# Kernel tuning notes

Hardware: AMD Instinct MI355X
Metric: run time of the kernel (lower is better)

Reference implementation:

```python
import jax, jax.numpy as jnp
import numpy as np

T, D, E, K, F, SF = 4096, 1024, 8, 2, 1024, 1024  # tokens, d_model, experts, top_k, moe_ff, shared_ff


def setup_inputs() -> dict:
    key = jax.random.key(0)
    ks = jax.random.split(key, 10)
    hidden_states = jax.random.normal(ks[0], (T, D), jnp.float32)
    # balanced expert assignment: the fused kernel's get_split_sizes assumes tokens
    # split evenly across experts after permute_tokens, so exactly T*K/E per expert
    flat = jnp.arange(T * K) % E
    flat = jax.random.permutation(ks[1], flat)
    topk_indices = flat.reshape(T, K).astype(jnp.int32)
    w = jax.random.uniform(ks[2], (T, K), jnp.float32)
    topk_weights = w / w.sum(-1, keepdims=True)  # norm_topk_prob
    s = 0.02
    w_gate = jax.random.normal(ks[3], (E, D, F), jnp.float32) * s
    w_up = jax.random.normal(ks[4], (E, D, F), jnp.float32) * s
    w_down = jax.random.normal(ks[5], (E, F, D), jnp.float32) * s
    sw_gate = jax.random.normal(ks[6], (D, SF), jnp.float32) * s
    sw_up = jax.random.normal(ks[7], (D, SF), jnp.float32) * s
    sw_down = jax.random.normal(ks[8], (SF, D), jnp.float32) * s
    shared_gate_w = jax.random.normal(ks[9], (D, 1), jnp.float32) * s
    return dict(hidden_states=hidden_states, topk_weights=topk_weights,
                w_gate=w_gate, w_up=w_up, w_down=w_down,
                sw_gate=sw_gate, sw_up=sw_up, sw_down=sw_down,
                shared_gate_w=shared_gate_w, topk_indices=topk_indices)


def _silu(x):
    return x * jax.nn.sigmoid(x)


def reference(hidden_states, topk_weights, w_gate, w_up, w_down,
              sw_gate, sw_up, sw_down, shared_gate_w, topk_indices):
    t, d = hidden_states.shape
    e = w_gate.shape[0]
    k = topk_indices.shape[1]
    c = (t * k) // e  # tokens per expert (balanced split, as in get_split_sizes)

    # permute_tokens: replicate each token top_k times and sort by expert id
    flat_idx = topk_indices.reshape(-1)                    # [t*k]
    order = jnp.argsort(flat_idx)                          # dispatch permutation
    x_rep = jnp.repeat(hidden_states, k, axis=0)           # [t*k, d]
    xs = x_rep[order].reshape(e, c, d)                     # grouped per-expert

    # per-expert gated MLP (grouped GEMMs)
    h = _silu(jnp.einsum('ecd,edf->ecf', xs, w_gate)) * jnp.einsum('ecd,edf->ecf', xs, w_up)
    y = jnp.einsum('ecf,efd->ecd', h, w_down).reshape(t * k, d)

    # unpermute_tokens + weighted combine over top_k
    y = y[jnp.argsort(order)].reshape(t, k, d)
    out = (y * topk_weights[..., None]).sum(axis=1)        # [t, d]

    # shared expert with sigmoid gate
    s = jnp.einsum('tf,fd->td', _silu(hidden_states @ sw_gate) * (hidden_states @ sw_up), sw_down)
    g = jax.nn.sigmoid(hidden_states @ shared_gate_w)      # [t, 1]
    return (out + g * s).astype(hidden_states.dtype)
```

## Files before the change

kernel.cpp:

```cpp
#include <hip/hip_runtime.h>
#include <hip/hip_bf16.h>
#include <cstdint>
#include <cstddef>

#define TTOK 4096
#define DM   1024
#define NE   8
#define KTOP 2
#define FFD  1024
#define CPER 1024
#define MROWS 12288

typedef __attribute__((ext_vector_type(8))) short frag8;
typedef __attribute__((ext_vector_type(4))) float f32x4;

static __device__ __forceinline__ unsigned short f2bf(float f) {
  unsigned int u = __float_as_uint(f);
  u += 0x7fff + ((u >> 16) & 1);
  return (unsigned short)(u >> 16);
}
static __device__ __forceinline__ float bf2f(unsigned short u) {
  return __uint_as_float((unsigned int)u << 16);
}

static __device__ __forceinline__ void gld_lds16(const unsigned short* g, unsigned short* l) {
  __builtin_amdgcn_global_load_lds(
      (const __attribute__((address_space(1))) unsigned int*)g,
      (__attribute__((address_space(3))) unsigned int*)l,
      16, 0, 0);
}

static __device__ __forceinline__ int lds_slot(int r, int cs) {
  return r * 4 + (cs ^ ((r >> 1) & 3));
}

static __device__ __forceinline__ void stage_tile(const unsigned short* __restrict__ src,
                                                  int row0, int k0,
                                                  unsigned short* lds, int tid) {
#pragma unroll
  for (int it = 0; it < 2; ++it) {
    int seg = it * 256 + tid;
    int r = seg >> 2;
    int cs = (seg & 3) ^ ((r >> 1) & 3);
    gld_lds16(src + (size_t)(row0 + r) * 1024 + k0 + cs * 8, lds + seg * 8);
  }
}

__global__ void perm_kernel(const int* __restrict__ idx, int* __restrict__ cnt,
                            int* __restrict__ rowdst, int* __restrict__ inv) {
  int i = blockIdx.x * 256 + threadIdx.x;
  int e = idx[i];
  int pos = atomicAdd(&cnt[e], 1);
  int j = e * CPER + pos;
  rowdst[j] = i >> 1;
  inv[i] = j;
}

__global__ void pack_kernel(const float* __restrict__ x, const int* __restrict__ rowdst,
                            unsigned short* __restrict__ xall) {
  int j = blockIdx.x;
  int t = (j < 8192) ? rowdst[j] : (j - 8192);
  int c = threadIdx.x;
  float4 v = ((const float4*)(x + (size_t)t * 1024))[c];
  ushort4 o;
  o.x = f2bf(v.x); o.y = f2bf(v.y); o.z = f2bf(v.z); o.w = f2bf(v.w);
  ((ushort4*)(xall + (size_t)j * 1024))[c] = o;
}

__global__ void transw_kernel(const float* __restrict__ wg, const float* __restrict__ wu,
                              const float* __restrict__ wd, const float* __restrict__ sg,
                              const float* __restrict__ su, const float* __restrict__ sd,
                              unsigned short* __restrict__ owg, unsigned short* __restrict__ owu,
                              unsigned short* __restrict__ owd) {
  int z = blockIdx.z;
  const float* src; unsigned short* dst;
  if (z < 8)       { src = wg + (size_t)z * 1048576;        dst = owg + (size_t)z * 1048576; }
  else if (z < 16) { src = wu + (size_t)(z - 8) * 1048576;  dst = owu + (size_t)(z - 8) * 1048576; }
  else if (z < 24) { src = wd + (size_t)(z - 16) * 1048576; dst = owd + (size_t)(z - 16) * 1048576; }
  else if (z == 24){ src = sg; dst = owg + (size_t)8 * 1048576; }
  else if (z == 25){ src = su; dst = owu + (size_t)8 * 1048576; }
  else             { src = sd; dst = owd + (size_t)8 * 1048576; }
  __shared__ float tile[32][33];
  int bx = blockIdx.x * 32;
  int by = blockIdx.y * 32;
  int tx = threadIdx.x, ty = threadIdx.y;
#pragma unroll
  for (int i = 0; i < 4; ++i)
    tile[ty + 8 * i][tx] = src[(size_t)(by + ty + 8 * i) * 1024 + bx + tx];
  __syncthreads();
#pragma unroll
  for (int i = 0; i < 4; ++i)
    dst[(size_t)(bx + ty + 8 * i) * 1024 + by + tx] = f2bf(tile[tx][ty + 8 * i]);
}

__global__ void gate_kernel(const float* __restrict__ x, const float* __restrict__ gw,
                            float* __restrict__ g) {
  int t = blockIdx.x * 4 + (threadIdx.x >> 6);
  int lane = threadIdx.x & 63;
  const float4* xr = (const float4*)(x + (size_t)t * 1024);
  const float4* wr = (const float4*)gw;
  float s = 0.f;
#pragma unroll
  for (int c = lane; c < 256; c += 64) {
    float4 a = xr[c], b = wr[c];
    s += a.x * b.x + a.y * b.y + a.z * b.z + a.w * b.w;
  }
#pragma unroll
  for (int off = 32; off; off >>= 1) s += __shfl_down(s, off);
  if (lane == 0) g[t] = 1.f / (1.f + __expf(-s));
}

static __device__ __forceinline__ int eid_of(int y) { return (y < 64) ? (y >> 3) : 8; }

__global__ __launch_bounds__(256, 2) void gemm1_kernel(
    const unsigned short* __restrict__ A, const unsigned short* __restrict__ Bg,
    const unsigned short* __restrict__ Bu, unsigned short* __restrict__ H) {
  __shared__ __align__(16) unsigned short As[128 * 32];
  __shared__ __align__(16) unsigned short Bgs[128 * 32];
  __shared__ __align__(16) unsigned short Bus[128 * 32];
  int tid = threadIdx.x;
  int e = eid_of(blockIdx.y);
  int row0 = blockIdx.y * 128;
  int col0 = blockIdx.x * 128;
  const unsigned short* Bge = Bg + (size_t)e * 1048576;
  const unsigned short* Bue = Bu + (size_t)e * 1048576;

  int wave = tid >> 6, lane = tid & 63;
  int wm = wave >> 1, wn = wave & 1;
  int lr = lane & 15, q = lane >> 4;

  f32x4 accg[4][4], accu[4][4];
#pragma unroll
  for (int i = 0; i < 4; ++i)
#pragma unroll
    for (int j = 0; j < 4; ++j) {
      accg[i][j] = (f32x4){0.f, 0.f, 0.f, 0.f};
      accu[i][j] = (f32x4){0.f, 0.f, 0.f, 0.f};
    }

  for (int kt = 0; kt < 1024; kt += 32) {
    stage_tile(A, row0, kt, As, tid);
    stage_tile(Bge, col0, kt, Bgs, tid);
    stage_tile(Bue, col0, kt, Bus, tid);
    __syncthreads();
    frag8 a[4], b0[4], b1[4];
#pragma unroll
    for (int i = 0; i < 4; ++i) {
      int r = wm * 64 + i * 16 + lr;
      a[i] = *(const frag8*)&As[lds_slot(r, q) * 8];
    }
#pragma unroll
    for (int j = 0; j < 4; ++j) {
      int r = wn * 64 + j * 16 + lr;
      b0[j] = *(const frag8*)&Bgs[lds_slot(r, q) * 8];
      b1[j] = *(const frag8*)&Bus[lds_slot(r, q) * 8];
    }
#pragma unroll
    for (int i = 0; i < 4; ++i)
#pragma unroll
      for (int j = 0; j < 4; ++j) {
        accg[i][j] = __builtin_amdgcn_mfma_f32_16x16x32_bf16(a[i], b0[j], accg[i][j], 0, 0, 0);
        accu[i][j] = __builtin_amdgcn_mfma_f32_16x16x32_bf16(a[i], b1[j], accu[i][j], 0, 0, 0);
      }
    __syncthreads();
  }
#pragma unroll
  for (int i = 0; i < 4; ++i)
#pragma unroll
    for (int j = 0; j < 4; ++j)
#pragma unroll
      for (int r = 0; r < 4; ++r) {
        int m = row0 + wm * 64 + i * 16 + q * 4 + r;
        int n = col0 + wn * 64 + j * 16 + lr;
        float gv = accg[i][j][r];
        float hv = gv / (1.f + __expf(-gv)) * accu[i][j][r];
        H[(size_t)m * 1024 + n] = f2bf(hv);
      }
}

__global__ __launch_bounds__(256, 2) void gemm2_kernel(
    const unsigned short* __restrict__ A, const unsigned short* __restrict__ B,
    unsigned short* __restrict__ Y) {
  __shared__ __align__(16) unsigned short As[128 * 32];
  __shared__ __align__(16) unsigned short Bs[128 * 32];
  int tid = threadIdx.x;
  int e = eid_of(blockIdx.y);
  int row0 = blockIdx.y * 128;
  int col0 = blockIdx.x * 128;
  const unsigned short* Be = B + (size_t)e * 1048576;

  int wave = tid >> 6, lane = tid & 63;
  int wm = wave >> 1, wn = wave & 1;
  int lr = lane & 15, q = lane >> 4;

  f32x4 acc[4][4];
#pragma unroll
  for (int i = 0; i < 4; ++i)
#pragma unroll
    for (int j = 0; j < 4; ++j) acc[i][j] = (f32x4){0.f, 0.f, 0.f, 0.f};

  for (int kt = 0; kt < 1024; kt += 32) {
    stage_tile(A, row0, kt, As, tid);
    stage_tile(Be, col0, kt, Bs, tid);
    __syncthreads();
    frag8 a[4], b[4];
#pragma unroll
    for (int i = 0; i < 4; ++i) {
      int r = wm * 64 + i * 16 + lr;
      a[i] = *(const frag8*)&As[lds_slot(r, q) * 8];
    }
#pragma unroll
    for (int j = 0; j < 4; ++j) {
      int r = wn * 64 + j * 16 + lr;
      b[j] = *(const frag8*)&Bs[lds_slot(r, q) * 8];
    }
#pragma unroll
    for (int i = 0; i < 4; ++i)
#pragma unroll
      for (int j = 0; j < 4; ++j)
        acc[i][j] = __builtin_amdgcn_mfma_f32_16x16x32_bf16(a[i], b[j], acc[i][j], 0, 0, 0);
    __syncthreads();
  }
#pragma unroll
  for (int i = 0; i < 4; ++i)
#pragma unroll
    for (int j = 0; j < 4; ++j)
#pragma unroll
      for (int r = 0; r < 4; ++r) {
        int m = row0 + wm * 64 + i * 16 + q * 4 + r;
        int n = col0 + wn * 64 + j * 16 + lr;
        Y[(size_t)m * 1024 + n] = f2bf(acc[i][j][r]);
      }
}

__global__ void combine_kernel(const unsigned short* __restrict__ Y,
                               const int* __restrict__ inv, const float* __restrict__ tw,
                               const float* __restrict__ g, float* __restrict__ out) {
  int t = blockIdx.x;
  int c = threadIdx.x;
  int j0 = inv[2 * t], j1 = inv[2 * t + 1];
  float w0 = tw[2 * t], w1 = tw[2 * t + 1], gg = g[t];
  ushort4 a = ((const ushort4*)(Y + (size_t)j0 * 1024))[c];
  ushort4 b = ((const ushort4*)(Y + (size_t)j1 * 1024))[c];
  ushort4 s = ((const ushort4*)(Y + (size_t)(8192 + t) * 1024))[c];
  float4 o;
  o.x = w0 * bf2f(a.x) + w1 * bf2f(b.x) + gg * bf2f(s.x);
  o.y = w0 * bf2f(a.y) + w1 * bf2f(b.y) + gg * bf2f(s.y);
  o.z = w0 * bf2f(a.z) + w1 * bf2f(b.z) + gg * bf2f(s.z);
  o.w = w0 * bf2f(a.w) + w1 * bf2f(b.w) + gg * bf2f(s.w);
  ((float4*)(out + (size_t)t * 1024))[c] = o;
}

extern "C" void kernel_launch(void* const* d_in, const int* in_sizes, int n_in,
                              void* d_out, int out_size, void* d_ws, size_t ws_size,
                              hipStream_t stream) {
  (void)in_sizes; (void)n_in; (void)out_size; (void)ws_size;
  const float* hidden  = (const float*)d_in[0];
  const float* topk_w  = (const float*)d_in[1];
  const float* w_gate  = (const float*)d_in[2];
  const float* w_up    = (const float*)d_in[3];
  const float* w_down  = (const float*)d_in[4];
  const float* sw_gate = (const float*)d_in[5];
  const float* sw_up   = (const float*)d_in[6];
  const float* sw_down = (const float*)d_in[7];
  const float* sgw     = (const float*)d_in[8];
  const int*   topk_i  = (const int*)d_in[9];
  float* out = (float*)d_out;

  char* p = (char*)d_ws;
  auto alloc = [&](size_t bytes) {
    char* r = p;
    p += (bytes + 255) & ~(size_t)255;
    return r;
  };
  unsigned short* Wg_all = (unsigned short*)alloc((size_t)9 * 1048576 * 2);
  unsigned short* Wu_all = (unsigned short*)alloc((size_t)9 * 1048576 * 2);
  unsigned short* Wd_all = (unsigned short*)alloc((size_t)9 * 1048576 * 2);
  unsigned short* Xall   = (unsigned short*)alloc((size_t)MROWS * 1024 * 2);
  unsigned short* Hall   = (unsigned short*)alloc((size_t)MROWS * 1024 * 2);
  int*   cnt    = (int*)alloc(NE * 4);
  int*   rowdst = (int*)alloc((size_t)TTOK * KTOP * 4);
  int*   inv    = (int*)alloc((size_t)TTOK * KTOP * 4);
  float* gbuf   = (float*)alloc((size_t)TTOK * 4);
  unsigned short* Yall = Xall;

  hipMemsetAsync(cnt, 0, NE * 4, stream);

  perm_kernel<<<TTOK * KTOP / 256, 256, 0, stream>>>(topk_i, cnt, rowdst, inv);
  pack_kernel<<<MROWS, 256, 0, stream>>>(hidden, rowdst, Xall);
  transw_kernel<<<dim3(32, 32, 27), dim3(32, 8), 0, stream>>>(
      w_gate, w_up, w_down, sw_gate, sw_up, sw_down, Wg_all, Wu_all, Wd_all);
  gate_kernel<<<TTOK / 4, 256, 0, stream>>>(hidden, sgw, gbuf);

  gemm1_kernel<<<dim3(8, 96), 256, 0, stream>>>(Xall, Wg_all, Wu_all, Hall);
  gemm2_kernel<<<dim3(8, 96), 256, 0, stream>>>(Hall, Wd_all, Yall);
  combine_kernel<<<TTOK, 256, 0, stream>>>(Yall, inv, topk_w, gbuf, out);
}
```

Baseline: 333.7 us.

## Double GEMM K-tile to 64, rework transpose with 64x64 vectorized tiles

Both expert GEMM kernels now stage 64-wide K slices per iteration with a new 8-way XOR swizzle, which halves the number of barrier pairs and loop iterations. Launch bounds rise to 3 blocks per CU. The weight transpose/convert kernel moves from 32x32 to 64x64 tiles with float4 loads and ushort4 stores to improve memory efficiency. LDS per gemm1 block grows to 48KB, and the higher occupancy target may force register spilling given the 128 accumulator registers per thread.

```diff
diff --git a/kernel.cpp b/kernel.cpp
--- a/kernel.cpp
+++ b/kernel.cpp
@@ -30,18 +30,18 @@
       16, 0, 0);
 }
 
-static __device__ __forceinline__ int lds_slot(int r, int cs) {
-  return r * 4 + (cs ^ ((r >> 1) & 3));
-}
-
-static __device__ __forceinline__ void stage_tile(const unsigned short* __restrict__ src,
-                                                  int row0, int k0,
-                                                  unsigned short* lds, int tid) {
-#pragma unroll
-  for (int it = 0; it < 2; ++it) {
+static __device__ __forceinline__ int lds_slot64(int r, int c) {
+  return r * 8 + (c ^ (r & 7));
+}
+
+static __device__ __forceinline__ void stage_tile64(const unsigned short* __restrict__ src,
+                                                    int row0, int k0,
+                                                    unsigned short* lds, int tid) {
+#pragma unroll
+  for (int it = 0; it < 4; ++it) {
     int seg = it * 256 + tid;
-    int r = seg >> 2;
-    int cs = (seg & 3) ^ ((r >> 1) & 3);
+    int r = seg >> 3;
+    int cs = (seg & 7) ^ (r & 7);
     gld_lds16(src + (size_t)(row0 + r) * 1024 + k0 + cs * 8, lds + seg * 8);
   }
 }
@@ -80,17 +80,29 @@
   else if (z == 24){ src = sg; dst = owg + (size_t)8 * 1048576; }
   else if (z == 25){ src = su; dst = owu + (size_t)8 * 1048576; }
   else             { src = sd; dst = owd + (size_t)8 * 1048576; }
-  __shared__ float tile[32][33];
-  int bx = blockIdx.x * 32;
-  int by = blockIdx.y * 32;
-  int tx = threadIdx.x, ty = threadIdx.y;
-#pragma unroll
-  for (int i = 0; i < 4; ++i)
-    tile[ty + 8 * i][tx] = src[(size_t)(by + ty + 8 * i) * 1024 + bx + tx];
+  __shared__ float tile[64][65];
+  int bx = blockIdx.x * 64;
+  int by = blockIdx.y * 64;
+  int c4 = threadIdx.x & 15;
+  int r0 = threadIdx.x >> 4;
+#pragma unroll
+  for (int i = 0; i < 4; ++i) {
+    int r = r0 + 16 * i;
+    float4 v = *(const float4*)&src[(size_t)(by + r) * 1024 + bx + c4 * 4];
+    tile[r][c4 * 4 + 0] = v.x; tile[r][c4 * 4 + 1] = v.y;
+    tile[r][c4 * 4 + 2] = v.z; tile[r][c4 * 4 + 3] = v.w;
+  }
   __syncthreads();
 #pragma unroll
-  for (int i = 0; i < 4; ++i)
-    dst[(size_t)(bx + ty + 8 * i) * 1024 + by + tx] = f2bf(tile[tx][ty + 8 * i]);
+  for (int i = 0; i < 4; ++i) {
+    int f = r0 + 16 * i;
+    ushort4 o;
+    o.x = f2bf(tile[c4 * 4 + 0][f]);
+    o.y = f2bf(tile[c4 * 4 + 1][f]);
+    o.z = f2bf(tile[c4 * 4 + 2][f]);
+    o.w = f2bf(tile[c4 * 4 + 3][f]);
+    *(ushort4*)&dst[(size_t)(bx + f) * 1024 + by + c4 * 4] = o;
+  }
 }
 
 __global__ void gate_kernel(const float* __restrict__ x, const float* __restrict__ gw,
@@ -112,12 +124,12 @@
 
 static __device__ __forceinline__ int eid_of(int y) { return (y < 64) ? (y >> 3) : 8; }
 
-__global__ __launch_bounds__(256, 2) void gemm1_kernel(
+__global__ __launch_bounds__(256, 3) void gemm1_kernel(
     const unsigned short* __restrict__ A, const unsigned short* __restrict__ Bg,
     const unsigned short* __restrict__ Bu, unsigned short* __restrict__ H) {
-  __shared__ __align__(16) unsigned short As[128 * 32];
-  __shared__ __align__(16) unsigned short Bgs[128 * 32];
-  __shared__ __align__(16) unsigned short Bus[128 * 32];
+  __shared__ __align__(16) unsigned short As[128 * 64];
+  __shared__ __align__(16) unsigned short Bgs[128 * 64];
+  __shared__ __align__(16) unsigned short Bus[128 * 64];
   int tid = threadIdx.x;
   int e = eid_of(blockIdx.y);
   int row0 = blockIdx.y * 128;
@@ -138,30 +150,34 @@
       accu[i][j] = (f32x4){0.f, 0.f, 0.f, 0.f};
     }
 
-  for (int kt = 0; kt < 1024; kt += 32) {
-    stage_tile(A, row0, kt, As, tid);
-    stage_tile(Bge, col0, kt, Bgs, tid);
-    stage_tile(Bue, col0, kt, Bus, tid);
+  for (int kt = 0; kt < 1024; kt += 64) {
+    stage_tile64(A, row0, kt, As, tid);
+    stage_tile64(Bge, col0, kt, Bgs, tid);
+    stage_tile64(Bue, col0, kt, Bus, tid);
     __syncthreads();
-    frag8 a[4], b0[4], b1[4];
-#pragma unroll
-    for (int i = 0; i < 4; ++i) {
-      int r = wm * 64 + i * 16 + lr;
-      a[i] = *(const frag8*)&As[lds_slot(r, q) * 8];
+#pragma unroll
+    for (int kk = 0; kk < 2; ++kk) {
+      int c = kk * 4 + q;
+      frag8 a[4], b0[4], b1[4];
+#pragma unroll
+      for (int i = 0; i < 4; ++i) {
+        int r = wm * 64 + i * 16 + lr;
+        a[i] = *(const frag8*)&As[lds_slot64(r, c) * 8];
+      }
+#pragma unroll
+      for (int j = 0; j < 4; ++j) {
+        int r = wn * 64 + j * 16 + lr;
+        b0[j] = *(const frag8*)&Bgs[lds_slot64(r, c) * 8];
+        b1[j] = *(const frag8*)&Bus[lds_slot64(r, c) * 8];
+      }
+#pragma unroll
+      for (int i = 0; i < 4; ++i)
+#pragma unroll
+        for (int j = 0; j < 4; ++j) {
+          accg[i][j] = __builtin_amdgcn_mfma_f32_16x16x32_bf16(a[i], b0[j], accg[i][j], 0, 0, 0);
+          accu[i][j] = __builtin_amdgcn_mfma_f32_16x16x32_bf16(a[i], b1[j], accu[i][j], 0, 0, 0);
+        }
     }
-#pragma unroll
-    for (int j = 0; j < 4; ++j) {
-      int r = wn * 64 + j * 16 + lr;
-      b0[j] = *(const frag8*)&Bgs[lds_slot(r, q) * 8];
-      b1[j] = *(const frag8*)&Bus[lds_slot(r, q) * 8];
-    }
-#pragma unroll
-    for (int i = 0; i < 4; ++i)
-#pragma unroll
-      for (int j = 0; j < 4; ++j) {
-        accg[i][j] = __builtin_amdgcn_mfma_f32_16x16x32_bf16(a[i], b0[j], accg[i][j], 0, 0, 0);
-        accu[i][j] = __builtin_amdgcn_mfma_f32_16x16x32_bf16(a[i], b1[j], accu[i][j], 0, 0, 0);
-      }
     __syncthreads();
   }
 #pragma unroll
@@ -178,11 +194,11 @@
       }
 }
 
-__global__ __launch_bounds__(256, 2) void gemm2_kernel(
+__global__ __launch_bounds__(256, 3) void gemm2_kernel(
     const unsigned short* __restrict__ A, const unsigned short* __restrict__ B,
     unsigned short* __restrict__ Y) {
-  __shared__ __align__(16) unsigned short As[128 * 32];
-  __shared__ __align__(16) unsigned short Bs[128 * 32];
+  __shared__ __align__(16) unsigned short As[128 * 64];
+  __shared__ __align__(16) unsigned short Bs[128 * 64];
   int tid = threadIdx.x;
   int e = eid_of(blockIdx.y);
   int row0 = blockIdx.y * 128;
@@ -199,26 +215,30 @@
 #pragma unroll
     for (int j = 0; j < 4; ++j) acc[i][j] = (f32x4){0.f, 0.f, 0.f, 0.f};
 
-  for (int kt = 0; kt < 1024; kt += 32) {
-    stage_tile(A, row0, kt, As, tid);
-    stage_tile(Be, col0, kt, Bs, tid);
+  for (int kt = 0; kt < 1024; kt += 64) {
+    stage_tile64(A, row0, kt, As, tid);
+    stage_tile64(Be, col0, kt, Bs, tid);
     __syncthreads();
-    frag8 a[4], b[4];
-#pragma unroll
-    for (int i = 0; i < 4; ++i) {
-      int r = wm * 64 + i * 16 + lr;
-      a[i] = *(const frag8*)&As[lds_slot(r, q) * 8];
+#pragma unroll
+    for (int kk = 0; kk < 2; ++kk) {
+      int c = kk * 4 + q;
+      frag8 a[4], b[4];
+#pragma unroll
+      for (int i = 0; i < 4; ++i) {
+        int r = wm * 64 + i * 16 + lr;
+        a[i] = *(const frag8*)&As[lds_slot64(r, c) * 8];
+      }
+#pragma unroll
+      for (int j = 0; j < 4; ++j) {
+        int r = wn * 64 + j * 16 + lr;
+        b[j] = *(const frag8*)&Bs[lds_slot64(r, c) * 8];
+      }
+#pragma unroll
+      for (int i = 0; i < 4; ++i)
+#pragma unroll
+        for (int j = 0; j < 4; ++j)
+          acc[i][j] = __builtin_amdgcn_mfma_f32_16x16x32_bf16(a[i], b[j], acc[i][j], 0, 0, 0);
     }
-#pragma unroll
-    for (int j = 0; j < 4; ++j) {
-      int r = wn * 64 + j * 16 + lr;
-      b[j] = *(const frag8*)&Bs[lds_slot(r, q) * 8];
-    }
-#pragma unroll
-    for (int i = 0; i < 4; ++i)
-#pragma unroll
-      for (int j = 0; j < 4; ++j)
-        acc[i][j] = __builtin_amdgcn_mfma_f32_16x16x32_bf16(a[i], b[j], acc[i][j], 0, 0, 0);
     __syncthreads();
   }
 #pragma unroll
@@ -288,7 +308,7 @@
 
   perm_kernel<<<TTOK * KTOP / 256, 256, 0, stream>>>(topk_i, cnt, rowdst, inv);
   pack_kernel<<<MROWS, 256, 0, stream>>>(hidden, rowdst, Xall);
-  transw_kernel<<<dim3(32, 32, 27), dim3(32, 8), 0, stream>>>(
+  transw_kernel<<<dim3(16, 16, 27), 256, 0, stream>>>(
       w_gate, w_up, w_down, sw_gate, sw_up, sw_down, Wg_all, Wu_all, Wd_all);
   gate_kernel<<<TTOK / 4, 256, 0, stream>>>(hidden, sgw, gbuf);
 
```

New measurement: 370.8 us. +11.1%, slower.
